# Performance work log

Hardware: AMD Instinct MI355X
Metric: run time of the kernel (lower is better)

Reference implementation:

```python
import jax, jax.numpy as jnp
import numpy as np
import math

B, S, H, NH, DH, FF, L = 2, 1024, 768, 12, 64, 3072, 4
LN_EPS = 1e-12


def _layer_norm(x, g, b):
    m = jnp.mean(x, axis=-1, keepdims=True)
    v = jnp.mean(jnp.square(x - m), axis=-1, keepdims=True)
    return (x - m) * jax.lax.rsqrt(v + LN_EPS) * g + b


def _gelu(x):
    # BERT erf-based gelu: x * 0.5 * (1 + erf(x / sqrt(2)))
    return x * 0.5 * (1.0 + jax.lax.erf(x / jnp.sqrt(jnp.asarray(2.0, x.dtype))))


def setup_inputs() -> dict:
    key = jax.random.key(0)
    ks = jax.random.split(key, 10)
    init = lambda k, shape: (jax.random.normal(k, shape, jnp.float32) * 0.02)
    inp = {
        'x': jax.random.normal(ks[0], (B, S, H), jnp.float32),
        'mask': jax.random.randint(ks[1], (B, S, S), 0, 2).astype(jnp.int32),
        'Wq': init(ks[2], (L, H, H)), 'bq': jnp.zeros((L, H), jnp.float32),
        'Wk': init(ks[3], (L, H, H)), 'bk': jnp.zeros((L, H), jnp.float32),
        'Wv': init(ks[4], (L, H, H)), 'bv': jnp.zeros((L, H), jnp.float32),
        'Wao': init(ks[5], (L, H, H)), 'bao': jnp.zeros((L, H), jnp.float32),
        'g1': jnp.ones((L, H), jnp.float32), 'b1': jnp.zeros((L, H), jnp.float32),
        'Wi': init(ks[6], (L, H, FF)), 'bi': jnp.zeros((L, FF), jnp.float32),
        'Wfo': init(ks[7], (L, FF, H)), 'bfo': jnp.zeros((L, H), jnp.float32),
        'g2': jnp.ones((L, H), jnp.float32), 'b2': jnp.zeros((L, H), jnp.float32),
    }
    return inp


def reference(x, mask, Wq, bq, Wk, bk, Wv, bv, Wao, bao, g1, b1, Wi, bi, Wfo, bfo, g2, b2):
    # additive mask: (1 - mask) * -10000, broadcast over heads -> [B,1,S,S]
    adder = (1.0 - mask.astype(x.dtype))[:, None, :, :] * -10000.0
    scale = 1.0 / math.sqrt(DH)

    def block(h, p):
        (wq, bq_, wk, bk_, wv, bv_, wao, bao_, g1_, b1_, wi, bi_, wfo, bfo_, g2_, b2_) = p
        q = (h @ wq + bq_).reshape(B, S, NH, DH)
        k = (h @ wk + bk_).reshape(B, S, NH, DH)
        v = (h @ wv + bv_).reshape(B, S, NH, DH)
        scores = jnp.einsum('bqhd,bkhd->bhqk', q, k) * scale + adder
        probs = jax.nn.softmax(scores, axis=-1)
        ctx = jnp.einsum('bhqk,bkhd->bqhd', probs, v).reshape(B, S, H)
        attn_out = _layer_norm(ctx @ wao + bao_ + h, g1_, b1_)
        inter = _gelu(attn_out @ wi + bi_)
        out = _layer_norm(inter @ wfo + bfo_ + attn_out, g2_, b2_)
        return out, None

    params = (Wq, bq, Wk, bk, Wv, bv, Wao, bao, g1, b1, Wi, bi, Wfo, bfo, g2, b2)
    out, _ = jax.lax.scan(block, x, params)
    return out
```

## Files before the change

kernel.cpp:

```cpp
#include <hip/hip_runtime.h>
#include <math.h>

#define B_  2
#define S_  1024
#define H_  768
#define NH_ 12
#define DH_ 64
#define FF_ 3072
#define L_  4

typedef short v8s __attribute__((ext_vector_type(8)));
typedef float v4f __attribute__((ext_vector_type(4)));

static __device__ __forceinline__ unsigned short f2bf(float f) {
    unsigned int u = __float_as_uint(f);
    unsigned int r = (u + 0x7fffu + ((u >> 16) & 1u)) >> 16;
    return (unsigned short)r;
}

__global__ void conv_bf16_k(const float* __restrict__ in, unsigned short* __restrict__ out, int n) {
    int i = blockIdx.x * 256 + threadIdx.x;
    if (i < n) out[i] = f2bf(in[i]);
}

__global__ __launch_bounds__(256) void transpose_convert(
    const float* __restrict__ W, unsigned short* __restrict__ Wt,
    int K, int N, size_t in_lstride, size_t out_lstride)
{
    __shared__ float tile[32][33];
    const int l = blockIdx.z;
    const float* src = W + (size_t)l * in_lstride;
    unsigned short* dst = Wt + (size_t)l * out_lstride;
    const int k0 = blockIdx.x * 32;
    const int n0 = blockIdx.y * 32;
    const int t = threadIdx.x;
    const int tc = t & 31, tr = t >> 5;
#pragma unroll
    for (int i = 0; i < 4; ++i) {
        int r = tr + i * 8;
        tile[r][tc] = src[(size_t)(k0 + r) * N + n0 + tc];
    }
    __syncthreads();
#pragma unroll
    for (int i = 0; i < 4; ++i) {
        int r = tr + i * 8;
        dst[(size_t)(n0 + r) * K + k0 + tc] = f2bf(tile[tc][r]);
    }
}

template<int ACT, int OUT_BF, int HAS_RES, int NBIAS>
__global__ __launch_bounds__(256) void gemm_k(
    const unsigned short* __restrict__ A,
    const unsigned short* __restrict__ Bt,
    const float* __restrict__ b0,
    const float* __restrict__ b1,
    const float* __restrict__ b2,
    const float* __restrict__ res,
    void* __restrict__ out,
    int M, int N, int K)
{
    __shared__ __align__(16) unsigned short As[64][40];
    __shared__ __align__(16) unsigned short Bs[64][40];
    const int t = threadIdx.x;
    const int m0 = blockIdx.x * 64;
    const int n0 = blockIdx.y * 64;
    const int lane = t & 63;
    const int wave = t >> 6;
    const int wm = wave >> 1;
    const int wn = wave & 1;
    const int l15 = lane & 15;
    const int kr = (lane >> 4) * 8;

    v4f acc[2][2] = {};

    const int ar = t >> 2;
    const int ac = (t & 3) * 8;
    const size_t arowA = (size_t)(m0 + ar) * K + ac;
    const size_t arowB = (size_t)(n0 + ar) * K + ac;

    for (int k0 = 0; k0 < K; k0 += 32) {
        __syncthreads();
        *(uint4*)(&As[ar][ac]) = *(const uint4*)(&A[arowA + k0]);
        *(uint4*)(&Bs[ar][ac]) = *(const uint4*)(&Bt[arowB + k0]);
        __syncthreads();
        v8s av0 = *(const v8s*)(&As[wm * 32 + 0 + l15][kr]);
        v8s av1 = *(const v8s*)(&As[wm * 32 + 16 + l15][kr]);
        v8s bv0 = *(const v8s*)(&Bs[wn * 32 + 0 + l15][kr]);
        v8s bv1 = *(const v8s*)(&Bs[wn * 32 + 16 + l15][kr]);
        acc[0][0] = __builtin_amdgcn_mfma_f32_16x16x32_bf16(av0, bv0, acc[0][0], 0, 0, 0);
        acc[0][1] = __builtin_amdgcn_mfma_f32_16x16x32_bf16(av0, bv1, acc[0][1], 0, 0, 0);
        acc[1][0] = __builtin_amdgcn_mfma_f32_16x16x32_bf16(av1, bv0, acc[1][0], 0, 0, 0);
        acc[1][1] = __builtin_amdgcn_mfma_f32_16x16x32_bf16(av1, bv1, acc[1][1], 0, 0, 0);
    }

    const int rb = (lane >> 4) * 4;
#pragma unroll
    for (int fm = 0; fm < 2; ++fm)
#pragma unroll
        for (int fn = 0; fn < 2; ++fn)
#pragma unroll
            for (int i = 0; i < 4; ++i) {
                int row = m0 + wm * 32 + fm * 16 + rb + i;
                int col = n0 + wn * 32 + fn * 16 + l15;
                float v = acc[fm][fn][i];
                float bb;
                if (NBIAS == 3) {
                    int which = (col >= 1536) ? 2 : (col >= 768 ? 1 : 0);
                    const float* bp = (which == 0) ? b0 : ((which == 1) ? b1 : b2);
                    bb = bp[col - which * 768];
                } else {
                    bb = b0[col];
                }
                v += bb;
                if (HAS_RES) v += res[(size_t)row * N + col];
                if (ACT == 1) v = 0.5f * v * (1.0f + erff(v * 0.70710678118654752f));
                size_t oi = (size_t)row * N + col;
                if (OUT_BF) ((unsigned short*)out)[oi] = f2bf(v);
                else        ((float*)out)[oi] = v;
            }
}

__global__ __launch_bounds__(256) void ln_k(
    const float* __restrict__ in, const float* __restrict__ g, const float* __restrict__ be,
    float* __restrict__ outf, unsigned short* __restrict__ outb)
{
    const int row = blockIdx.x;
    const float* x = in + (size_t)row * H_;
    const int t = threadIdx.x;
    const int wave = t >> 6, lane = t & 63;
    float v0 = x[t], v1 = x[t + 256], v2 = x[t + 512];
    float s = v0 + v1 + v2;
    float s2 = v0 * v0 + v1 * v1 + v2 * v2;
#pragma unroll
    for (int o = 32; o; o >>= 1) { s += __shfl_xor(s, o); s2 += __shfl_xor(s2, o); }
    __shared__ float rs[4], rq[4];
    if (lane == 0) { rs[wave] = s; rq[wave] = s2; }
    __syncthreads();
    s  = rs[0] + rs[1] + rs[2] + rs[3];
    s2 = rq[0] + rq[1] + rq[2] + rq[3];
    const float mean = s * (1.0f / 768.0f);
    float var = s2 * (1.0f / 768.0f) - mean * mean;
    var = fmaxf(var, 0.0f);
    const float inv = rsqrtf(var + 1e-12f);
#pragma unroll
    for (int i = 0; i < 3; ++i) {
        int c = t + i * 256;
        float vv = (i == 0) ? v0 : ((i == 1) ? v1 : v2);
        float y = (vv - mean) * inv * g[c] + be[c];
        outf[(size_t)row * H_ + c] = y;
        outb[(size_t)row * H_ + c] = f2bf(y);
    }
}

__global__ __launch_bounds__(256) void fattn_k(
    const unsigned short* __restrict__ qkv,
    const int* __restrict__ mask,
    unsigned short* __restrict__ ctx)
{
    const int qt = blockIdx.x, h = blockIdx.y, b = blockIdx.z;
    const int q0 = qt * 64;
    const int t = threadIdx.x;
    const int wave = t >> 6, lane = t & 63;
    const int l15 = lane & 15;
    const int kr8 = (lane >> 4) * 8;
    const int rb  = (lane >> 4) * 4;
    const int wq0 = wave * 16;

    __shared__ __align__(16) unsigned short Ks[64][72];
    __shared__ __align__(16) unsigned short Ps[64][72];
    __shared__ __align__(16) unsigned short VtL[64 * 64];

    const size_t rstr = 2304;
    const unsigned short* base = qkv + (size_t)b * S_ * rstr + h * 64;

    v8s qf0, qf1;
    {
        const unsigned short* qp = base + (size_t)(q0 + wq0 + l15) * rstr + kr8;
        qf0 = *(const v8s*)qp;
        qf1 = *(const v8s*)(qp + 32);
    }

    const int skp = t >> 3;
    const int sch = t & 7;
    const int sd0 = sch * 8;

    float m_[4], l_[4];
    v4f accO[4];
#pragma unroll
    for (int i = 0; i < 4; ++i) { m_[i] = -3.0e38f; l_[i] = 0.f; }
#pragma unroll
    for (int f = 0; f < 4; ++f) accO[f] = (v4f){0.f, 0.f, 0.f, 0.f};

    const int* mrow[4];
#pragma unroll
    for (int i = 0; i < 4; ++i)
        mrow[i] = mask + ((size_t)(b * S_) + q0 + wq0 + rb + i) * S_;

    for (int kt = 0; kt < 16; ++kt) {
        const int k0 = kt * 64;
        __syncthreads();
        {
            const unsigned short* kp = base + 768 + (size_t)(k0 + skp) * rstr + sd0;
            v8s kv0 = *(const v8s*)kp;
            v8s kv1 = *(const v8s*)(kp + 32 * rstr);
            *(v8s*)&Ks[skp][sd0] = kv0;
            *(v8s*)&Ks[skp + 32][sd0] = kv1;
            const unsigned short* vp = base + 1536 + (size_t)(k0 + 2 * skp) * rstr + sd0;
            v8s va = *(const v8s*)vp;
            v8s vb = *(const v8s*)(vp + rstr);
#pragma unroll
            for (int j = 0; j < 8; ++j) {
                const int d = sd0 + j;
                const int sw = ((d & 7) ^ (d >> 3)) << 3;
                unsigned int pk = ((unsigned int)(unsigned short)vb[j] << 16) | (unsigned short)va[j];
                *(unsigned int*)&VtL[(size_t)d * 64 + ((2 * skp) ^ sw)] = pk;
            }
        }
        __syncthreads();

        v4f s4[4];
#pragma unroll
        for (int f = 0; f < 4; ++f) s4[f] = (v4f){0.f, 0.f, 0.f, 0.f};
#pragma unroll
        for (int ks = 0; ks < 2; ++ks) {
            v8s qv = ks ? qf1 : qf0;
#pragma unroll
            for (int f = 0; f < 4; ++f) {
                v8s kf = *(const v8s*)&Ks[f * 16 + l15][ks * 32 + kr8];
                s4[f] = __builtin_amdgcn_mfma_f32_16x16x32_bf16(qv, kf, s4[f], 0, 0, 0);
            }
        }

        float p[4][4];
        float mx[4];
#pragma unroll
        for (int i = 0; i < 4; ++i) mx[i] = -3.0e38f;
#pragma unroll
        for (int f = 0; f < 4; ++f)
#pragma unroll
            for (int i = 0; i < 4; ++i) {
                int mval = mrow[i][k0 + f * 16 + l15];
                float v = s4[f][i] * 0.125f + (mval ? 0.f : -10000.f);
                p[f][i] = v;
                mx[i] = fmaxf(mx[i], v);
            }
#pragma unroll
        for (int o = 8; o; o >>= 1)
#pragma unroll
            for (int i = 0; i < 4; ++i) mx[i] = fmaxf(mx[i], __shfl_xor(mx[i], o));
        float corr[4], rsum[4];
#pragma unroll
        for (int i = 0; i < 4; ++i) {
            float mn = fmaxf(m_[i], mx[i]);
            corr[i] = __expf(m_[i] - mn);
            m_[i] = mn;
            rsum[i] = 0.f;
        }
#pragma unroll
        for (int f = 0; f < 4; ++f)
#pragma unroll
            for (int i = 0; i < 4; ++i) {
                float e = __expf(p[f][i] - m_[i]);
                p[f][i] = e;
                rsum[i] += e;
            }
#pragma unroll
        for (int o = 8; o; o >>= 1)
#pragma unroll
            for (int i = 0; i < 4; ++i) rsum[i] += __shfl_xor(rsum[i], o);
#pragma unroll
        for (int i = 0; i < 4; ++i) l_[i] = l_[i] * corr[i] + rsum[i];
#pragma unroll
        for (int f = 0; f < 4; ++f)
#pragma unroll
            for (int i = 0; i < 4; ++i) accO[f][i] *= corr[i];

#pragma unroll
        for (int f = 0; f < 4; ++f)
#pragma unroll
            for (int i = 0; i < 4; ++i)
                Ps[wq0 + rb + i][f * 16 + l15] = f2bf(p[f][i]);

#pragma unroll
        for (int ks = 0; ks < 2; ++ks) {
            v8s pf = *(const v8s*)&Ps[wq0 + l15][ks * 32 + kr8];
#pragma unroll
            for (int f = 0; f < 4; ++f) {
                const int d = f * 16 + l15;
                const int sw = ((d & 7) ^ (d >> 3)) << 3;
                v8s vf = *(const v8s*)&VtL[(size_t)d * 64 + ((ks * 32 + kr8) ^ sw)];
                accO[f] = __builtin_amdgcn_mfma_f32_16x16x32_bf16(pf, vf, accO[f], 0, 0, 0);
            }
        }
    }

#pragma unroll
    for (int f = 0; f < 4; ++f)
#pragma unroll
        for (int i = 0; i < 4; ++i) {
            float o = accO[f][i] / l_[i];
            size_t row = (size_t)(b * S_) + q0 + wq0 + rb + i;
            ctx[row * 768 + h * 64 + f * 16 + l15] = f2bf(o);
        }
}

extern "C" void kernel_launch(void* const* d_in, const int* in_sizes, int n_in,
                              void* d_out, int out_size, void* d_ws, size_t ws_size,
                              hipStream_t stream)
{
    const float* x   = (const float*)d_in[0];
    const int*   mask= (const int*)  d_in[1];
    const float* Wq  = (const float*)d_in[2];
    const float* bq  = (const float*)d_in[3];
    const float* Wk  = (const float*)d_in[4];
    const float* bk  = (const float*)d_in[5];
    const float* Wv  = (const float*)d_in[6];
    const float* bv  = (const float*)d_in[7];
    const float* Wao = (const float*)d_in[8];
    const float* bao = (const float*)d_in[9];
    const float* g1  = (const float*)d_in[10];
    const float* b1  = (const float*)d_in[11];
    const float* Wi  = (const float*)d_in[12];
    const float* bi  = (const float*)d_in[13];
    const float* Wfo = (const float*)d_in[14];
    const float* bfo = (const float*)d_in[15];
    const float* g2  = (const float*)d_in[16];
    const float* b2  = (const float*)d_in[17];
    float* out = (float*)d_out;

    const int M = B_ * S_;
    char* base = (char*)d_ws;
    size_t off = 0;
    auto alloc = [&](size_t bytes) -> char* {
        char* p = base + off;
        off = (off + bytes + 255) & ~(size_t)255;
        return p;
    };

    unsigned short* WqkvT = (unsigned short*)alloc((size_t)L_ * 2304 * 768 * 2);
    unsigned short* WaoT  = (unsigned short*)alloc((size_t)L_ * 768 * 768 * 2);
    unsigned short* WiT   = (unsigned short*)alloc((size_t)L_ * 3072 * 768 * 2);
    unsigned short* WfoT  = (unsigned short*)alloc((size_t)L_ * 768 * 3072 * 2);
    unsigned short* h_bf  = (unsigned short*)alloc((size_t)M * 768 * 2);
    unsigned short* qkvbf = (unsigned short*)alloc((size_t)M * 2304 * 2);
    unsigned short* ctxbf = (unsigned short*)alloc((size_t)M * 768 * 2);
    float* t1             = (float*)alloc((size_t)M * 768 * 4);
    float* attnf          = (float*)alloc((size_t)M * 768 * 4);
    unsigned short* attnbf= (unsigned short*)alloc((size_t)M * 768 * 2);
    float* hcur           = (float*)alloc((size_t)M * 768 * 4);
    unsigned short* interbf = (unsigned short*)alloc((size_t)M * FF_ * 2);

    dim3 tb(256);
    transpose_convert<<<dim3(24, 24, L_), tb, 0, stream>>>(Wq,  WqkvT + 0,          768,  768, (size_t)768 * 768,  (size_t)2304 * 768);
    transpose_convert<<<dim3(24, 24, L_), tb, 0, stream>>>(Wk,  WqkvT + 768 * 768,  768,  768, (size_t)768 * 768,  (size_t)2304 * 768);
    transpose_convert<<<dim3(24, 24, L_), tb, 0, stream>>>(Wv,  WqkvT + 1536 * 768, 768,  768, (size_t)768 * 768,  (size_t)2304 * 768);
    transpose_convert<<<dim3(24, 24, L_), tb, 0, stream>>>(Wao, WaoT,               768,  768, (size_t)768 * 768,  (size_t)768 * 768);
    transpose_convert<<<dim3(24, 96, L_), tb, 0, stream>>>(Wi,  WiT,                768, 3072, (size_t)768 * 3072, (size_t)3072 * 768);
    transpose_convert<<<dim3(96, 24, L_), tb, 0, stream>>>(Wfo, WfoT,              3072,  768, (size_t)3072 * 768, (size_t)768 * 3072);

    conv_bf16_k<<<(M * 768 + 255) / 256, 256, 0, stream>>>(x, h_bf, M * 768);

    const float* hres = x;
    for (int l = 0; l < L_; ++l) {
        gemm_k<0, 1, 0, 3><<<dim3(32, 36), tb, 0, stream>>>(
            h_bf, WqkvT + (size_t)l * 2304 * 768,
            bq + l * 768, bk + l * 768, bv + l * 768, nullptr, qkvbf, M, 2304, 768);
        fattn_k<<<dim3(S_ / 64, NH_, B_), tb, 0, stream>>>(qkvbf, mask, ctxbf);
        gemm_k<0, 0, 1, 1><<<dim3(32, 12), tb, 0, stream>>>(
            ctxbf, WaoT + (size_t)l * 768 * 768,
            bao + l * 768, nullptr, nullptr, hres, t1, M, 768, 768);
        ln_k<<<M, tb, 0, stream>>>(t1, g1 + l * 768, b1 + l * 768, attnf, attnbf);
        gemm_k<1, 1, 0, 1><<<dim3(32, 48), tb, 0, stream>>>(
            attnbf, WiT + (size_t)l * 3072 * 768,
            bi + l * 3072, nullptr, nullptr, nullptr, interbf, M, 3072, 768);
        gemm_k<0, 0, 1, 1><<<dim3(32, 12), tb, 0, stream>>>(
            interbf, WfoT + (size_t)l * 3072 * 768,
            bfo + l * 768, nullptr, nullptr, attnf, t1, M, 768, 3072);
        float* of = (l == L_ - 1) ? out : hcur;
        ln_k<<<M, tb, 0, stream>>>(t1, g2 + l * 768, b2 + l * 768, of, h_bf);
        hres = hcur;
    }
}
```

Measured before the change: 815.7 us.

## Enlarge GEMM tiles with direct-to-LDS loads, split-K, and split-KV attention

GEMM tiles grow from 64x64 to 128x128 with a 4x4 MFMA fragment grid per wave. Operands load straight into swizzled LDS through global_load_lds, and the two N=768 GEMMs use 2-way split-K whose partial sums are added inside the layernorm kernel. Attention runs 512 threads that split the key range in two, register-prefetch the next K/V tile and merge the two halves' softmax state at the end. The int mask is pre-converted once per launch to a bf16 additive mask. Risks include fewer blocks for the smaller GEMMs, extra partial-sum traffic, and reusing the qkv buffer as the split-K scratch.

```diff
diff --git a/kernel.cpp b/kernel.cpp
--- a/kernel.cpp
+++ b/kernel.cpp
@@ -17,10 +17,22 @@
     unsigned int r = (u + 0x7fffu + ((u >> 16) & 1u)) >> 16;
     return (unsigned short)r;
 }
+static __device__ __forceinline__ float bf2f(unsigned short u) {
+    return __uint_as_float((unsigned int)u << 16);
+}
+
+#define GLOAD16(g, l) __builtin_amdgcn_global_load_lds( \
+    (const __attribute__((address_space(1))) unsigned int*)(g), \
+    (__attribute__((address_space(3))) unsigned int*)(l), 16, 0, 0)
 
 __global__ void conv_bf16_k(const float* __restrict__ in, unsigned short* __restrict__ out, int n) {
     int i = blockIdx.x * 256 + threadIdx.x;
     if (i < n) out[i] = f2bf(in[i]);
+}
+
+__global__ void maskconv_k(const int* __restrict__ m, unsigned short* __restrict__ o, int n) {
+    int i = blockIdx.x * 256 + threadIdx.x;
+    if (i < n) o[i] = m[i] ? (unsigned short)0u : (unsigned short)0xC61Cu;
 }
 
 __global__ __launch_bounds__(256) void transpose_convert(
@@ -48,7 +60,7 @@
     }
 }
 
-template<int ACT, int OUT_BF, int HAS_RES, int NBIAS>
+template<int ACT, int OUT_BF, int NBIAS, int SPLIT>
 __global__ __launch_bounds__(256) void gemm_k(
     const unsigned short* __restrict__ A,
     const unsigned short* __restrict__ Bt,
@@ -56,79 +68,105 @@
     const float* __restrict__ b1,
     const float* __restrict__ b2,
     const float* __restrict__ res,
-    void* __restrict__ out,
-    int M, int N, int K)
+    void* __restrict__ out0,
+    float* __restrict__ out1,
+    int M, int N, int K, int klen)
 {
-    __shared__ __align__(16) unsigned short As[64][40];
-    __shared__ __align__(16) unsigned short Bs[64][40];
+    __shared__ __align__(16) unsigned short As[128 * 32];
+    __shared__ __align__(16) unsigned short Bs[128 * 32];
     const int t = threadIdx.x;
-    const int m0 = blockIdx.x * 64;
-    const int n0 = blockIdx.y * 64;
+    const int m0 = blockIdx.x * 128;
+    const int n0 = blockIdx.y * 128;
+    const int kz = SPLIT ? blockIdx.z : 0;
+    const int kstart = kz * klen;
     const int lane = t & 63;
-    const int wave = t >> 6;
-    const int wm = wave >> 1;
-    const int wn = wave & 1;
+    const int w = t >> 6;
+    const int wm = w >> 1, wn = w & 1;
     const int l15 = lane & 15;
-    const int kr = (lane >> 4) * 8;
-
-    v4f acc[2][2] = {};
-
-    const int ar = t >> 2;
-    const int ac = (t & 3) * 8;
-    const size_t arowA = (size_t)(m0 + ar) * K + ac;
-    const size_t arowB = (size_t)(n0 + ar) * K + ac;
-
-    for (int k0 = 0; k0 < K; k0 += 32) {
+    const int kr8 = (lane >> 4) * 8;
+
+    const int rg = lane >> 2;
+    const int cg = lane & 3;
+    const int rA0 = (w * 2 + 0) * 16 + rg;
+    const int rA1 = (w * 2 + 1) * 16 + rg;
+    const int cs0 = (cg ^ ((rA0 >> 1) & 3)) * 8;
+    const int cs1 = (cg ^ ((rA1 >> 1) & 3)) * 8;
+    const unsigned short* gA0 = A  + (size_t)(m0 + rA0) * K + kstart + cs0;
+    const unsigned short* gA1 = A  + (size_t)(m0 + rA1) * K + kstart + cs1;
+    const unsigned short* gB0 = Bt + (size_t)(n0 + rA0) * K + kstart + cs0;
+    const unsigned short* gB1 = Bt + (size_t)(n0 + rA1) * K + kstart + cs1;
+    unsigned short* lA0 = &As[(w * 2 + 0) * 16 * 32];
+    unsigned short* lA1 = &As[(w * 2 + 1) * 16 * 32];
+    unsigned short* lB0 = &Bs[(w * 2 + 0) * 16 * 32];
+    unsigned short* lB1 = &Bs[(w * 2 + 1) * 16 * 32];
+
+    const int abase = l15 * 32 + (kr8 ^ (((l15 >> 1) & 3) << 3));
+
+    v4f acc[4][4] = {};
+
+    for (int k0 = 0; k0 < klen; k0 += 32) {
         __syncthreads();
-        *(uint4*)(&As[ar][ac]) = *(const uint4*)(&A[arowA + k0]);
-        *(uint4*)(&Bs[ar][ac]) = *(const uint4*)(&Bt[arowB + k0]);
+        GLOAD16(gA0 + k0, lA0);
+        GLOAD16(gA1 + k0, lA1);
+        GLOAD16(gB0 + k0, lB0);
+        GLOAD16(gB1 + k0, lB1);
         __syncthreads();
-        v8s av0 = *(const v8s*)(&As[wm * 32 + 0 + l15][kr]);
-        v8s av1 = *(const v8s*)(&As[wm * 32 + 16 + l15][kr]);
-        v8s bv0 = *(const v8s*)(&Bs[wn * 32 + 0 + l15][kr]);
-        v8s bv1 = *(const v8s*)(&Bs[wn * 32 + 16 + l15][kr]);
-        acc[0][0] = __builtin_amdgcn_mfma_f32_16x16x32_bf16(av0, bv0, acc[0][0], 0, 0, 0);
-        acc[0][1] = __builtin_amdgcn_mfma_f32_16x16x32_bf16(av0, bv1, acc[0][1], 0, 0, 0);
-        acc[1][0] = __builtin_amdgcn_mfma_f32_16x16x32_bf16(av1, bv0, acc[1][0], 0, 0, 0);
-        acc[1][1] = __builtin_amdgcn_mfma_f32_16x16x32_bf16(av1, bv1, acc[1][1], 0, 0, 0);
+        v8s a[4], b[4];
+#pragma unroll
+        for (int i = 0; i < 4; ++i) a[i] = *(const v8s*)&As[(wm * 64 + i * 16) * 32 + abase];
+#pragma unroll
+        for (int i = 0; i < 4; ++i) b[i] = *(const v8s*)&Bs[(wn * 64 + i * 16) * 32 + abase];
+#pragma unroll
+        for (int fm = 0; fm < 4; ++fm)
+#pragma unroll
+            for (int fn = 0; fn < 4; ++fn)
+                acc[fm][fn] = __builtin_amdgcn_mfma_f32_16x16x32_bf16(a[fm], b[fn], acc[fm][fn], 0, 0, 0);
     }
 
     const int rb = (lane >> 4) * 4;
 #pragma unroll
-    for (int fm = 0; fm < 2; ++fm)
-#pragma unroll
-        for (int fn = 0; fn < 2; ++fn)
+    for (int fm = 0; fm < 4; ++fm)
+#pragma unroll
+        for (int fn = 0; fn < 4; ++fn)
 #pragma unroll
             for (int i = 0; i < 4; ++i) {
-                int row = m0 + wm * 32 + fm * 16 + rb + i;
-                int col = n0 + wn * 32 + fn * 16 + l15;
+                const int row = m0 + wm * 64 + fm * 16 + rb + i;
+                const int col = n0 + wn * 64 + fn * 16 + l15;
                 float v = acc[fm][fn][i];
-                float bb;
-                if (NBIAS == 3) {
-                    int which = (col >= 1536) ? 2 : (col >= 768 ? 1 : 0);
-                    const float* bp = (which == 0) ? b0 : ((which == 1) ? b1 : b2);
-                    bb = bp[col - which * 768];
+                const size_t oi = (size_t)row * N + col;
+                if (!SPLIT || kz == 0) {
+                    float bb;
+                    if (NBIAS == 3) {
+                        int which = (col >= 1536) ? 2 : (col >= 768 ? 1 : 0);
+                        const float* bp = (which == 0) ? b0 : ((which == 1) ? b1 : b2);
+                        bb = bp[col - which * 768];
+                    } else {
+                        bb = b0[col];
+                    }
+                    v += bb;
+                    if (res) v += res[oi];
+                    if (ACT == 1) v = 0.5f * v * (1.0f + erff(v * 0.70710678118654752f));
+                    if (OUT_BF) ((unsigned short*)out0)[oi] = f2bf(v);
+                    else        ((float*)out0)[oi] = v;
                 } else {
-                    bb = b0[col];
+                    out1[oi] = v;
                 }
-                v += bb;
-                if (HAS_RES) v += res[(size_t)row * N + col];
-                if (ACT == 1) v = 0.5f * v * (1.0f + erff(v * 0.70710678118654752f));
-                size_t oi = (size_t)row * N + col;
-                if (OUT_BF) ((unsigned short*)out)[oi] = f2bf(v);
-                else        ((float*)out)[oi] = v;
             }
 }
 
 __global__ __launch_bounds__(256) void ln_k(
-    const float* __restrict__ in, const float* __restrict__ g, const float* __restrict__ be,
+    const float* __restrict__ ina, const float* __restrict__ inb,
+    const float* __restrict__ g, const float* __restrict__ be,
     float* __restrict__ outf, unsigned short* __restrict__ outb)
 {
     const int row = blockIdx.x;
-    const float* x = in + (size_t)row * H_;
+    const float* xa = ina + (size_t)row * H_;
+    const float* xb = inb + (size_t)row * H_;
     const int t = threadIdx.x;
     const int wave = t >> 6, lane = t & 63;
-    float v0 = x[t], v1 = x[t + 256], v2 = x[t + 512];
+    float v0 = xa[t] + xb[t];
+    float v1 = xa[t + 256] + xb[t + 256];
+    float v2 = xa[t + 512] + xb[t + 512];
     float s = v0 + v1 + v2;
     float s2 = v0 * v0 + v1 * v1 + v2 * v2;
 #pragma unroll
@@ -152,23 +190,25 @@
     }
 }
 
-__global__ __launch_bounds__(256) void fattn_k(
+__global__ __launch_bounds__(512) void fattn_k(
     const unsigned short* __restrict__ qkv,
-    const int* __restrict__ mask,
+    const unsigned short* __restrict__ madd,
     unsigned short* __restrict__ ctx)
 {
     const int qt = blockIdx.x, h = blockIdx.y, b = blockIdx.z;
     const int q0 = qt * 64;
     const int t = threadIdx.x;
-    const int wave = t >> 6, lane = t & 63;
+    const int w = t >> 6, lane = t & 63;
+    const int half = w >> 2, w4 = w & 3;
     const int l15 = lane & 15;
     const int kr8 = (lane >> 4) * 8;
     const int rb  = (lane >> 4) * 4;
-    const int wq0 = wave * 16;
-
-    __shared__ __align__(16) unsigned short Ks[64][72];
-    __shared__ __align__(16) unsigned short Ps[64][72];
-    __shared__ __align__(16) unsigned short VtL[64 * 64];
+    const int wq0 = w4 * 16;
+
+    __shared__ __align__(16) unsigned char smem[53248];
+    unsigned short* KsH = (unsigned short*)(smem)         + (size_t)half * (64 * 72);
+    unsigned short* VtH = (unsigned short*)(smem + 18432) + (size_t)half * 4096;
+    unsigned short* PsH = (unsigned short*)(smem + 34816) + (size_t)half * (64 * 72);
 
     const size_t rstr = 2304;
     const unsigned short* base = qkv + (size_t)b * S_ * rstr + h * 64;
@@ -180,9 +220,12 @@
         qf1 = *(const v8s*)(qp + 32);
     }
 
-    const int skp = t >> 3;
-    const int sch = t & 7;
-    const int sd0 = sch * 8;
+    const int tl  = t & 255;
+    const int skp = tl >> 3;
+    const int sd0 = (tl & 7) * 8;
+    const unsigned short* kbase = base + 768  + (size_t)(half * 512 + skp) * rstr + sd0;
+    const unsigned short* vbase = base + 1536 + (size_t)(half * 512 + 2 * skp) * rstr + sd0;
+    const size_t kstep = (size_t)64 * rstr;
 
     float m_[4], l_[4];
     v4f accO[4];
@@ -191,29 +234,55 @@
 #pragma unroll
     for (int f = 0; f < 4; ++f) accO[f] = (v4f){0.f, 0.f, 0.f, 0.f};
 
-    const int* mrow[4];
+    const unsigned short* mrow[4];
 #pragma unroll
     for (int i = 0; i < 4; ++i)
-        mrow[i] = mask + ((size_t)(b * S_) + q0 + wq0 + rb + i) * S_;
-
-    for (int kt = 0; kt < 16; ++kt) {
+        mrow[i] = madd + ((size_t)(b * S_) + q0 + wq0 + rb + i) * S_ + half * 512;
+
+    v8s kA0, kA1, vA0, vA1, kB0, kB1, vB0, vB1;
+    kA0 = *(const v8s*)(kbase);
+    kA1 = *(const v8s*)(kbase + 32 * rstr);
+    vA0 = *(const v8s*)(vbase);
+    vA1 = *(const v8s*)(vbase + rstr);
+
+    for (int kt = 0; kt < 8; ++kt) {
         const int k0 = kt * 64;
         __syncthreads();
-        {
-            const unsigned short* kp = base + 768 + (size_t)(k0 + skp) * rstr + sd0;
-            v8s kv0 = *(const v8s*)kp;
-            v8s kv1 = *(const v8s*)(kp + 32 * rstr);
-            *(v8s*)&Ks[skp][sd0] = kv0;
-            *(v8s*)&Ks[skp + 32][sd0] = kv1;
-            const unsigned short* vp = base + 1536 + (size_t)(k0 + 2 * skp) * rstr + sd0;
-            v8s va = *(const v8s*)vp;
-            v8s vb = *(const v8s*)(vp + rstr);
+        if ((kt & 1) == 0) {
+            *(v8s*)&KsH[skp * 72 + sd0] = kA0;
+            *(v8s*)&KsH[(skp + 32) * 72 + sd0] = kA1;
 #pragma unroll
             for (int j = 0; j < 8; ++j) {
                 const int d = sd0 + j;
                 const int sw = ((d & 7) ^ (d >> 3)) << 3;
-                unsigned int pk = ((unsigned int)(unsigned short)vb[j] << 16) | (unsigned short)va[j];
-                *(unsigned int*)&VtL[(size_t)d * 64 + ((2 * skp) ^ sw)] = pk;
+                unsigned int pk = ((unsigned int)(unsigned short)vA1[j] << 16) | (unsigned short)vA0[j];
+                *(unsigned int*)&VtH[(size_t)d * 64 + ((2 * skp) ^ sw)] = pk;
+            }
+            if (kt < 7) {
+                const unsigned short* kp = kbase + (size_t)(kt + 1) * kstep;
+                const unsigned short* vp = vbase + (size_t)(kt + 1) * kstep;
+                kB0 = *(const v8s*)kp;
+                kB1 = *(const v8s*)(kp + 32 * rstr);
+                vB0 = *(const v8s*)vp;
+                vB1 = *(const v8s*)(vp + rstr);
+            }
+        } else {
+            *(v8s*)&KsH[skp * 72 + sd0] = kB0;
+            *(v8s*)&KsH[(skp + 32) * 72 + sd0] = kB1;
+#pragma unroll
+            for (int j = 0; j < 8; ++j) {
+                const int d = sd0 + j;
+                const int sw = ((d & 7) ^ (d >> 3)) << 3;
+                unsigned int pk = ((unsigned int)(unsigned short)vB1[j] << 16) | (unsigned short)vB0[j];
+                *(unsigned int*)&VtH[(size_t)d * 64 + ((2 * skp) ^ sw)] = pk;
+            }
+            if (kt < 7) {
+                const unsigned short* kp = kbase + (size_t)(kt + 1) * kstep;
+                const unsigned short* vp = vbase + (size_t)(kt + 1) * kstep;
+                kA0 = *(const v8s*)kp;
+                kA1 = *(const v8s*)(kp + 32 * rstr);
+                vA0 = *(const v8s*)vp;
+                vA1 = *(const v8s*)(vp + rstr);
             }
         }
         __syncthreads();
@@ -226,7 +295,7 @@
             v8s qv = ks ? qf1 : qf0;
 #pragma unroll
             for (int f = 0; f < 4; ++f) {
-                v8s kf = *(const v8s*)&Ks[f * 16 + l15][ks * 32 + kr8];
+                v8s kf = *(const v8s*)&KsH[(f * 16 + l15) * 72 + ks * 32 + kr8];
                 s4[f] = __builtin_amdgcn_mfma_f32_16x16x32_bf16(qv, kf, s4[f], 0, 0, 0);
             }
         }
@@ -239,8 +308,7 @@
         for (int f = 0; f < 4; ++f)
 #pragma unroll
             for (int i = 0; i < 4; ++i) {
-                int mval = mrow[i][k0 + f * 16 + l15];
-                float v = s4[f][i] * 0.125f + (mval ? 0.f : -10000.f);
+                float v = s4[f][i] * 0.125f + bf2f(mrow[i][k0 + f * 16 + l15]);
                 p[f][i] = v;
                 mx[i] = fmaxf(mx[i], v);
             }
@@ -279,29 +347,55 @@
         for (int f = 0; f < 4; ++f)
 #pragma unroll
             for (int i = 0; i < 4; ++i)
-                Ps[wq0 + rb + i][f * 16 + l15] = f2bf(p[f][i]);
+                PsH[(wq0 + rb + i) * 72 + f * 16 + l15] = f2bf(p[f][i]);
 
 #pragma unroll
         for (int ks = 0; ks < 2; ++ks) {
-            v8s pf = *(const v8s*)&Ps[wq0 + l15][ks * 32 + kr8];
+            v8s pf = *(const v8s*)&PsH[(wq0 + l15) * 72 + ks * 32 + kr8];
 #pragma unroll
             for (int f = 0; f < 4; ++f) {
                 const int d = f * 16 + l15;
                 const int sw = ((d & 7) ^ (d >> 3)) << 3;
-                v8s vf = *(const v8s*)&VtL[(size_t)d * 64 + ((ks * 32 + kr8) ^ sw)];
+                v8s vf = *(const v8s*)&VtH[(size_t)d * 64 + ((ks * 32 + kr8) ^ sw)];
                 accO[f] = __builtin_amdgcn_mfma_f32_16x16x32_bf16(pf, vf, accO[f], 0, 0, 0);
             }
         }
     }
 
-#pragma unroll
-    for (int f = 0; f < 4; ++f)
+    __syncthreads();
+    float* Mb = (float*)smem;
+    const int mstr = 26;
+    if (half == 1) {
+        float* p = Mb + ((size_t)(w4 * 64 + lane)) * mstr;
+#pragma unroll
+        for (int i = 0; i < 4; ++i) { p[i] = m_[i]; p[4 + i] = l_[i]; }
+#pragma unroll
+        for (int f = 0; f < 4; ++f)
+#pragma unroll
+            for (int i = 0; i < 4; ++i) p[8 + f * 4 + i] = accO[f][i];
+    }
+    __syncthreads();
+    if (half == 0) {
+        const float* p = Mb + ((size_t)(w4 * 64 + lane)) * mstr;
+        float c0[4], c1[4];
 #pragma unroll
         for (int i = 0; i < 4; ++i) {
-            float o = accO[f][i] / l_[i];
-            size_t row = (size_t)(b * S_) + q0 + wq0 + rb + i;
-            ctx[row * 768 + h * 64 + f * 16 + l15] = f2bf(o);
+            float m1 = p[i], l1 = p[4 + i];
+            float mm = fmaxf(m_[i], m1);
+            c0[i] = __expf(m_[i] - mm);
+            c1[i] = __expf(m1 - mm);
+            l_[i] = l_[i] * c0[i] + l1 * c1[i];
+            m_[i] = mm;
         }
+#pragma unroll
+        for (int f = 0; f < 4; ++f)
+#pragma unroll
+            for (int i = 0; i < 4; ++i) {
+                float o = (accO[f][i] * c0[i] + p[8 + f * 4 + i] * c1[i]) / l_[i];
+                size_t row = (size_t)(b * S_) + q0 + wq0 + rb + i;
+                ctx[row * 768 + h * 64 + f * 16 + l15] = f2bf(o);
+            }
+    }
 }
 
 extern "C" void kernel_launch(void* const* d_in, const int* in_sizes, int n_in,
@@ -329,10 +423,10 @@
     float* out = (float*)d_out;
 
     const int M = B_ * S_;
-    char* base = (char*)d_ws;
+    char* basep = (char*)d_ws;
     size_t off = 0;
     auto alloc = [&](size_t bytes) -> char* {
-        char* p = base + off;
+        char* p = basep + off;
         off = (off + bytes + 255) & ~(size_t)255;
         return p;
     };
@@ -344,11 +438,12 @@
     unsigned short* h_bf  = (unsigned short*)alloc((size_t)M * 768 * 2);
     unsigned short* qkvbf = (unsigned short*)alloc((size_t)M * 2304 * 2);
     unsigned short* ctxbf = (unsigned short*)alloc((size_t)M * 768 * 2);
-    float* t1             = (float*)alloc((size_t)M * 768 * 4);
+    float* t1a            = (float*)alloc((size_t)M * 768 * 4);
     float* attnf          = (float*)alloc((size_t)M * 768 * 4);
     unsigned short* attnbf= (unsigned short*)alloc((size_t)M * 768 * 2);
-    float* hcur           = (float*)alloc((size_t)M * 768 * 4);
     unsigned short* interbf = (unsigned short*)alloc((size_t)M * FF_ * 2);
+    unsigned short* madd  = (unsigned short*)alloc((size_t)B_ * S_ * S_ * 2);
+    float* t1b = (float*)(void*)qkvbf;
 
     dim3 tb(256);
     transpose_convert<<<dim3(24, 24, L_), tb, 0, stream>>>(Wq,  WqkvT + 0,          768,  768, (size_t)768 * 768,  (size_t)2304 * 768);
@@ -359,25 +454,25 @@
     transpose_convert<<<dim3(96, 24, L_), tb, 0, stream>>>(Wfo, WfoT,              3072,  768, (size_t)3072 * 768, (size_t)768 * 3072);
 
     conv_bf16_k<<<(M * 768 + 255) / 256, 256, 0, stream>>>(x, h_bf, M * 768);
+    maskconv_k<<<(B_ * S_ * S_ + 255) / 256, 256, 0, stream>>>(mask, madd, B_ * S_ * S_);
 
     const float* hres = x;
     for (int l = 0; l < L_; ++l) {
-        gemm_k<0, 1, 0, 3><<<dim3(32, 36), tb, 0, stream>>>(
+        gemm_k<0, 1, 3, 0><<<dim3(16, 18), tb, 0, stream>>>(
             h_bf, WqkvT + (size_t)l * 2304 * 768,
-            bq + l * 768, bk + l * 768, bv + l * 768, nullptr, qkvbf, M, 2304, 768);
-        fattn_k<<<dim3(S_ / 64, NH_, B_), tb, 0, stream>>>(qkvbf, mask, ctxbf);
-        gemm_k<0, 0, 1, 1><<<dim3(32, 12), tb, 0, stream>>>(
+            bq + l * 768, bk + l * 768, bv + l * 768, nullptr, qkvbf, nullptr, M, 2304, 768, 768);
+        fattn_k<<<dim3(S_ / 64, NH_, B_), dim3(512), 0, stream>>>(qkvbf, madd, ctxbf);
+        gemm_k<0, 0, 1, 1><<<dim3(16, 6, 2), tb, 0, stream>>>(
             ctxbf, WaoT + (size_t)l * 768 * 768,
-            bao + l * 768, nullptr, nullptr, hres, t1, M, 768, 768);
-        ln_k<<<M, tb, 0, stream>>>(t1, g1 + l * 768, b1 + l * 768, attnf, attnbf);
-        gemm_k<1, 1, 0, 1><<<dim3(32, 48), tb, 0, stream>>>(
+            bao + l * 768, nullptr, nullptr, hres, t1a, t1b, M, 768, 768, 384);
+        ln_k<<<M, tb, 0, stream>>>(t1a, t1b, g1 + l * 768, b1 + l * 768, attnf, attnbf);
+        gemm_k<1, 1, 1, 0><<<dim3(16, 24), tb, 0, stream>>>(
             attnbf, WiT + (size_t)l * 3072 * 768,
-            bi + l * 3072, nullptr, nullptr, nullptr, interbf, M, 3072, 768);
-        gemm_k<0, 0, 1, 1><<<dim3(32, 12), tb, 0, stream>>>(
+            bi + l * 3072, nullptr, nullptr, nullptr, interbf, nullptr, M, 3072, 768, 768);
+        gemm_k<0, 0, 1, 1><<<dim3(16, 6, 2), tb, 0, stream>>>(
             interbf, WfoT + (size_t)l * 3072 * 768,
-            bfo + l * 768, nullptr, nullptr, attnf, t1, M, 768, 3072);
-        float* of = (l == L_ - 1) ? out : hcur;
-        ln_k<<<M, tb, 0, stream>>>(t1, g2 + l * 768, b2 + l * 768, of, h_bf);
-        hres = hcur;
-    }
-}
+            bfo + l * 768, nullptr, nullptr, attnf, t1a, t1b, M, 768, 3072, 1536);
+        ln_k<<<M, tb, 0, stream>>>(t1a, t1b, g2 + l * 768, b2 + l * 768, out, h_bf);
+        hres = out;
+    }
+}
```

Measured after the change: 1.015 ms. +24.4%, slower.
